# Performance work log

Hardware: AMD Instinct MI355X
Metric: run time of the kernel (lower is better)

The kernel has to match this reference:

```python
import jax, jax.numpy as jnp
import numpy as np

N, E = 50000, 800000
F_IN, F_EMB1, F_EMB2, F_HID, F_OUT = 128, 512, 128, 1024, 64


def _linear_params(k, fan_in, fan_out):
    s = 1.0 / np.sqrt(fan_in)
    kw, kb = jax.random.split(k)
    W = jax.random.uniform(kw, (fan_in, fan_out), jnp.float32, -s, s)
    b = jax.random.uniform(kb, (fan_out,), jnp.float32, -s, s)
    return W, b


def setup_inputs() -> dict:
    key = jax.random.key(0)
    ks = jax.random.split(key, 8)
    x = jax.random.normal(ks[0], (N, F_IN), jnp.float32)
    src = jax.random.randint(ks[1], (E,), 0, N)
    dst = jax.random.randint(ks[2], (E,), 0, N)
    edge_index = jnp.stack([src, dst])  # [2, E]
    edge_weight = jax.random.uniform(ks[3], (E,), jnp.float32)  # positive weights
    W1, b1 = _linear_params(ks[4], F_IN, F_EMB1)
    W2, b2 = _linear_params(ks[5], F_EMB1, F_EMB2)
    W3, b3 = _linear_params(ks[6], F_EMB2, F_HID)
    W4, b4 = _linear_params(ks[7], F_HID, F_OUT)
    return dict(x=x, edge_index=edge_index, edge_weight=edge_weight,
                W1=W1, b1=b1, W2=W2, b2=b2, W3=W3, b3=b3, W4=W4, b4=b4)


def gcn_conv(x, src, dst, w, W, b):
    """PyG GCNConv: transform, then sym-normalized weighted aggregation with self-loops.
    out = D^{-1/2} (A_w + I) D^{-1/2} (x W) + b,  deg = scatter(w @ dst) + 1."""
    n = x.shape[0]
    h = x @ W  # [N, F_out]
    deg = jax.ops.segment_sum(w, dst, num_segments=n) + 1.0  # +1 for self-loop weight
    dinv = jax.lax.rsqrt(deg)
    norm = dinv[src] * w * dinv[dst]  # [E]
    agg = jax.ops.segment_sum(norm[:, None] * h[src], dst, num_segments=n)
    agg = agg + h / deg[:, None]  # self-loop: dinv[i]*1*dinv[i] * h[i]
    return agg + b


def reference(x, edge_index, edge_weight, W1, b1, W2, b2, W3, b3, W4, b4):
    src, dst = edge_index[0], edge_index[1]
    h = jax.nn.relu(gcn_conv(x, src, dst, edge_weight, W1, b1))
    # graph_normalization=False -> identity; dropout is identity in eval mode
    h = jax.nn.relu(gcn_conv(h, src, dst, edge_weight, W2, b2))
    h = jax.nn.relu(h @ W3 + b3)
    out = jax.nn.relu(h @ W4 + b4)
    return out
```

## Files before the change

kernel.cpp:

```cpp
#include <hip/hip_runtime.h>


#define ELLW 64

typedef short bf16x8 __attribute__((ext_vector_type(8)));
typedef float f32x4 __attribute__((ext_vector_type(4)));

__device__ __forceinline__ unsigned short f2b(float f) {
    unsigned u = __builtin_bit_cast(unsigned, f);
    unsigned r = (u + 0x7FFFu + ((u >> 16) & 1u)) >> 16;
    return (unsigned short)r;
}
__device__ __forceinline__ float b2f(unsigned short u) {
    return __builtin_bit_cast(float, (unsigned)u << 16);
}

__global__ void k_setup(const float* __restrict__ x,
                        const float* __restrict__ W1, const float* __restrict__ W2,
                        const float* __restrict__ W3, const float* __restrict__ W4,
                        unsigned short* __restrict__ W1t, unsigned short* __restrict__ W2t,
                        unsigned short* __restrict__ W3t, unsigned short* __restrict__ W4t,
                        unsigned short* __restrict__ xb,
                        const int* __restrict__ src, const int* __restrict__ dst,
                        const float* __restrict__ ew, int* __restrict__ cnt,
                        int2* __restrict__ s_edge, int Nn, int E) {
    int b = blockIdx.x;
    if (b < 3125) {
        int e = b * 256 + threadIdx.x;
        if (e < E) {
            int d = dst[e];
            int2 rec = make_int2(src[e], __builtin_bit_cast(int, ew[e]));
            int slot = atomicAdd(&cnt[d], 1);
            if (slot < ELLW) s_edge[(size_t)d * ELLW + slot] = rec;
        }
    } else if (b < 4405) {
        int i = (b - 3125) * 256 + threadIdx.x;
        if (i < 65536) {
            int k = i >> 9, n = i & 511;
            W1t[n * 128 + k] = f2b(W1[i]);
        } else if (i < 131072) {
            int j = i - 65536; int k = j >> 7, n = j & 127;
            W2t[n * 512 + k] = f2b(W2[j]);
        } else if (i < 262144) {
            int j = i - 131072; int k = j >> 10, n = j & 1023;
            W3t[n * 128 + k] = f2b(W3[j]);
        } else {
            int j = i - 262144; int k = j >> 6, n = j & 63;
            W4t[n * 1024 + k] = f2b(W4[j]);
        }
    } else {
        int i = (b - 4405) * 256 + threadIdx.x;
        if (i < Nn * 32) {
            float4 v = ((const float4*)x)[i];
            ushort4 o;
            o.x = f2b(v.x); o.y = f2b(v.y); o.z = f2b(v.z); o.w = f2b(v.w);
            ((ushort4*)xb)[i] = o;
        }
    }
}

__global__ __launch_bounds__(256) void k_deg(const int2* __restrict__ s_edge,
                                             const int* __restrict__ cnt,
                                             float* __restrict__ dinv, int Nn) {
    int node = blockIdx.x * 4 + (threadIdx.x >> 6);
    if (node >= Nn) return;
    int lane = threadIdx.x & 63;
    int c = min(cnt[node], ELLW);
    float s = 0.0f;
    if (lane < c) s = __builtin_bit_cast(float, s_edge[(size_t)node * ELLW + lane].y);
    #pragma unroll
    for (int d = 32; d > 0; d >>= 1) s += __shfl_down(s, d);
    if (lane == 0) dinv[node] = rsqrtf(1.0f + s);
}

template <bool FIRST, bool BIAS_RELU>
__global__ __launch_bounds__(256) void k_gather(
    const unsigned short* __restrict__ Xb, int2* __restrict__ s_edge,
    const int* __restrict__ cnt, const float* __restrict__ dinv,
    const float* __restrict__ bias, unsigned short* __restrict__ outb, int Nn) {
    int node = blockIdx.x * 4 + (threadIdx.x >> 6);
    if (node >= Nn) return;
    int lane = threadIdx.x & 63;
    float di = dinv[node];
    float dii = di * di;
    ushort2 sv = ((const ushort2*)(Xb + (size_t)node * 128))[lane];
    float ax = b2f(sv.x) * dii, ay = b2f(sv.y) * dii;

    int c = min(cnt[node], ELLW);
    size_t base = (size_t)node * ELLW;
    int sreg = 0;
    float nv = 0.0f;
    if (lane < c) {
        int2 rec = s_edge[base + lane];
        sreg = rec.x;
        if (FIRST) {
            float wv = __builtin_bit_cast(float, rec.y);
            nv = dinv[sreg] * wv * di;
            ((int*)s_edge)[2 * (base + lane) + 1] = __builtin_bit_cast(int, nv);
        } else {
            nv = __builtin_bit_cast(float, rec.y);
        }
    }

    int j = 0;
    for (; j + 8 <= c; j += 8) {
        int s0 = __shfl(sreg, j),     s1 = __shfl(sreg, j + 1);
        int s2 = __shfl(sreg, j + 2), s3 = __shfl(sreg, j + 3);
        int s4 = __shfl(sreg, j + 4), s5 = __shfl(sreg, j + 5);
        int s6 = __shfl(sreg, j + 6), s7 = __shfl(sreg, j + 7);
        float n0 = __shfl(nv, j),     n1 = __shfl(nv, j + 1);
        float n2 = __shfl(nv, j + 2), n3 = __shfl(nv, j + 3);
        float n4 = __shfl(nv, j + 4), n5 = __shfl(nv, j + 5);
        float n6 = __shfl(nv, j + 6), n7 = __shfl(nv, j + 7);
        ushort2 r0 = ((const ushort2*)(Xb + (size_t)s0 * 128))[lane];
        ushort2 r1 = ((const ushort2*)(Xb + (size_t)s1 * 128))[lane];
        ushort2 r2 = ((const ushort2*)(Xb + (size_t)s2 * 128))[lane];
        ushort2 r3 = ((const ushort2*)(Xb + (size_t)s3 * 128))[lane];
        ushort2 r4 = ((const ushort2*)(Xb + (size_t)s4 * 128))[lane];
        ushort2 r5 = ((const ushort2*)(Xb + (size_t)s5 * 128))[lane];
        ushort2 r6 = ((const ushort2*)(Xb + (size_t)s6 * 128))[lane];
        ushort2 r7 = ((const ushort2*)(Xb + (size_t)s7 * 128))[lane];
        ax += n0 * b2f(r0.x) + n1 * b2f(r1.x) + n2 * b2f(r2.x) + n3 * b2f(r3.x);
        ay += n0 * b2f(r0.y) + n1 * b2f(r1.y) + n2 * b2f(r2.y) + n3 * b2f(r3.y);
        ax += n4 * b2f(r4.x) + n5 * b2f(r5.x) + n6 * b2f(r6.x) + n7 * b2f(r7.x);
        ay += n4 * b2f(r4.y) + n5 * b2f(r5.y) + n6 * b2f(r6.y) + n7 * b2f(r7.y);
    }
    for (; j < c; ++j) {
        int sj = __shfl(sreg, j);
        float nj = __shfl(nv, j);
        ushort2 r = ((const ushort2*)(Xb + (size_t)sj * 128))[lane];
        ax += nj * b2f(r.x);
        ay += nj * b2f(r.y);
    }

    if (BIAS_RELU) {
        float2 bv = ((const float2*)bias)[lane];
        ax = fmaxf(ax + bv.x, 0.0f);
        ay = fmaxf(ay + bv.y, 0.0f);
    }
    ushort2 o; o.x = f2b(ax); o.y = f2b(ay);
    ((ushort2*)(outb + (size_t)node * 128))[lane] = o;
}

template <int H, int OUTW, bool HAS_BO, bool OUT_BF16>
__global__ __launch_bounds__(256) void k_mlp(
    const unsigned short* __restrict__ A, const unsigned short* __restrict__ Wht,
    const unsigned short* __restrict__ Wot, const float* __restrict__ bh,
    const float* __restrict__ bo, void* __restrict__ out, int M) {
    constexpr int HC = H / 64;
    constexpr int NJ = OUTW / 16;
    constexpr int OW4 = OUTW / 32;
    __shared__ __align__(16) unsigned short Whs[64 * 128];
    __shared__ __align__(16) unsigned short Ps[128 * 64];
    __shared__ __align__(16) unsigned short Wos[OUTW * 64];
    const int tid = threadIdx.x, wave = tid >> 6, lane = tid & 63;
    const int lm = lane & 15, quad = lane >> 4;
    const int bm0 = blockIdx.x * 128;

    bf16x8 af[2][4];
    #pragma unroll
    for (int i = 0; i < 2; ++i) {
        int gr = bm0 + wave * 32 + i * 16 + lm;
        #pragma unroll
        for (int kb = 0; kb < 4; ++kb) af[i][kb] = bf16x8{0, 0, 0, 0, 0, 0, 0, 0};
        if (gr < M) {
            #pragma unroll
            for (int kb = 0; kb < 4; ++kb)
                af[i][kb] = *(const bf16x8*)(A + (size_t)gr * 128 + kb * 32 + quad * 8);
        }
    }

    #pragma unroll
    for (int u = 0; u < 4; ++u) {
        int idx = tid + u * 256; int r = idx >> 4, g = idx & 15;
        *(int4*)&Whs[r * 128 + ((g ^ (r & 15)) * 8)] =
            *(const int4*)(Wht + (size_t)r * 128 + g * 8);
    }
    #pragma unroll
    for (int u = 0; u < OW4; ++u) {
        int idx = tid + u * 256; int r = idx >> 3, g = idx & 7;
        *(int4*)&Wos[r * 64 + ((g ^ (r & 7)) * 8)] =
            *(const int4*)(Wot + (size_t)r * H + g * 8);
    }
    __syncthreads();

    f32x4 oacc[2][NJ] = {};
    for (int c = 0; c < HC; ++c) {
        f32x4 hacc[2][4] = {};
        #pragma unroll
        for (int kb = 0; kb < 4; ++kb) {
            bf16x8 bfr[4];
            #pragma unroll
            for (int j = 0; j < 4; ++j) {
                int r = j * 16 + lm, g = kb * 4 + quad;
                bfr[j] = *(const bf16x8*)&Whs[r * 128 + ((g ^ (r & 15)) * 8)];
            }
            #pragma unroll
            for (int i = 0; i < 2; ++i)
                #pragma unroll
                for (int j = 0; j < 4; ++j)
                    hacc[i][j] = __builtin_amdgcn_mfma_f32_16x16x32_bf16(
                        af[i][kb], bfr[j], hacc[i][j], 0, 0, 0);
        }

        #pragma unroll
        for (int i = 0; i < 2; ++i) {
            #pragma unroll
            for (int j = 0; j < 4; ++j) {
                int col = j * 16 + lm;
                float bv = bh[c * 64 + col];
                #pragma unroll
                for (int r4 = 0; r4 < 4; ++r4) {
                    int row = wave * 32 + i * 16 + quad * 4 + r4;
                    float o = fmaxf(hacc[i][j][r4] + bv, 0.0f);
                    Ps[row * 64 + (((col >> 3) ^ (row & 7)) * 8) + (col & 7)] = f2b(o);
                }
            }
        }

        #pragma unroll
        for (int kb = 0; kb < 2; ++kb) {
            bf16x8 pf[2];
            #pragma unroll
            for (int i = 0; i < 2; ++i) {
                int r = wave * 32 + i * 16 + lm, g = kb * 4 + quad;
                pf[i] = *(const bf16x8*)&Ps[r * 64 + ((g ^ (r & 7)) * 8)];
            }
            #pragma unroll
            for (int j = 0; j < NJ; ++j) {
                int r = j * 16 + lm, g = kb * 4 + quad;
                bf16x8 wf = *(const bf16x8*)&Wos[r * 64 + ((g ^ (r & 7)) * 8)];
                #pragma unroll
                for (int i = 0; i < 2; ++i)
                    oacc[i][j] = __builtin_amdgcn_mfma_f32_16x16x32_bf16(
                        pf[i], wf, oacc[i][j], 0, 0, 0);
            }
        }

        if (c + 1 < HC) {
            __syncthreads();
            #pragma unroll
            for (int u = 0; u < 4; ++u) {
                int idx = tid + u * 256; int r = idx >> 4, g = idx & 15;
                *(int4*)&Whs[r * 128 + ((g ^ (r & 15)) * 8)] =
                    *(const int4*)(Wht + (size_t)((c + 1) * 64 + r) * 128 + g * 8);
            }
            #pragma unroll
            for (int u = 0; u < OW4; ++u) {
                int idx = tid + u * 256; int r = idx >> 3, g = idx & 7;
                *(int4*)&Wos[r * 64 + ((g ^ (r & 7)) * 8)] =
                    *(const int4*)(Wot + (size_t)r * H + (c + 1) * 64 + g * 8);
            }
            __syncthreads();
        }
    }

    #pragma unroll
    for (int i = 0; i < 2; ++i) {
        #pragma unroll
        for (int j = 0; j < NJ; ++j) {
            int col = j * 16 + lm;
            float bv = HAS_BO ? bo[col] : 0.0f;
            #pragma unroll
            for (int r4 = 0; r4 < 4; ++r4) {
                int m = bm0 + wave * 32 + i * 16 + quad * 4 + r4;
                if (m < M) {
                    float o = oacc[i][j][r4];
                    if (HAS_BO) o = fmaxf(o + bv, 0.0f);
                    if (OUT_BF16)
                        ((unsigned short*)out)[(size_t)m * OUTW + col] = f2b(o);
                    else
                        ((float*)out)[(size_t)m * OUTW + col] = o;
                }
            }
        }
    }
}

static inline int cdiv(long a, long b) { return (int)((a + b - 1) / b); }

extern "C" void kernel_launch(void* const* d_in, const int* in_sizes, int n_in,
                              void* d_out, int out_size, void* d_ws, size_t ws_size,
                              hipStream_t stream) {
    const float* x  = (const float*)d_in[0];
    const int*   ei = (const int*)d_in[1];
    const float* ew = (const float*)d_in[2];
    const float* W1 = (const float*)d_in[3];
    const float* b1 = (const float*)d_in[4];
    const float* W2 = (const float*)d_in[5];
    const float* b2 = (const float*)d_in[6];
    const float* W3 = (const float*)d_in[7];
    const float* b3 = (const float*)d_in[8];
    const float* W4 = (const float*)d_in[9];
    const float* b4 = (const float*)d_in[10];
    const int Nn = in_sizes[0] / 128;
    const int E  = in_sizes[1] / 2;
    const int* src = ei;
    const int* dst = ei + E;

    char* ws = (char*)d_ws;
    size_t off_b = 0;
    auto alloc = [&](size_t bytes) -> void* {
        void* p = ws + off_b;
        off_b += (bytes + 255) & ~(size_t)255;
        return p;
    };
    float*          dinv   = (float*)alloc((size_t)Nn * 4);
    int*            cnt    = (int*)alloc((size_t)Nn * 4);
    int2*           s_edge = (int2*)alloc((size_t)Nn * ELLW * 8);
    unsigned short* W1t    = (unsigned short*)alloc(512 * 128 * 2);
    unsigned short* W2t    = (unsigned short*)alloc(128 * 512 * 2);
    unsigned short* W3t    = (unsigned short*)alloc(1024 * 128 * 2);
    unsigned short* W4t    = (unsigned short*)alloc(64 * 1024 * 2);
    unsigned short* xb     = (unsigned short*)alloc((size_t)Nn * 128 * 2);
    unsigned short* t2b    = (unsigned short*)alloc((size_t)Nn * 128 * 2);
    unsigned short* actb   = (unsigned short*)alloc((size_t)Nn * 128 * 2);
    float*          out    = (float*)d_out;

    hipMemsetAsync(cnt, 0, (size_t)Nn * 4, stream);
    k_setup<<<10655, 256, 0, stream>>>(x, W1, W2, W3, W4, W1t, W2t, W3t, W4t,
                                       xb, src, dst, ew, cnt, s_edge, Nn, E);
    k_deg<<<cdiv(Nn, 4), 256, 0, stream>>>(s_edge, cnt, dinv, Nn);

    k_gather<true, false><<<cdiv(Nn, 4), 256, 0, stream>>>(
        xb, s_edge, cnt, dinv, nullptr, actb, Nn);
    k_mlp<512, 128, false, true><<<cdiv(Nn, 128), 256, 0, stream>>>(
        actb, W1t, W2t, b1, nullptr, t2b, Nn);

    k_gather<false, true><<<cdiv(Nn, 4), 256, 0, stream>>>(
        t2b, s_edge, cnt, dinv, b2, actb, Nn);

    k_mlp<1024, 64, true, false><<<cdiv(Nn, 128), 256, 0, stream>>>(
        actb, W3t, W4t, b3, b4, out, Nn);
}
```

Baseline: 289.4 us.

## Factor symmetric normalization into node-side scaling and pack degree into count atomic

The edge-count atomic becomes a 64-bit atomic that also accumulates a fixed-point sum of edge weights, so the degree is available without a separate reduction over the edge lists. The D^{-1/2} factors are moved to node-side scaling: inputs are pre-scaled by dinv in a new degree/scale kernel, each gather multiplies its sum by dinv, and the first MLP scales its output by dinv. This removes the per-edge random dinv[src] lookup and the write-back of normalized weights in the first gather. The cost is an extra read-modify-write pass over xb, 64-bit atomics, fixed-point rounding of the degree, and an extra bf16 rounding of the pre-scaled input.

```diff
diff --git a/kernel.cpp b/kernel.cpp
--- a/kernel.cpp
+++ b/kernel.cpp
@@ -22,16 +22,22 @@
                         unsigned short* __restrict__ W3t, unsigned short* __restrict__ W4t,
                         unsigned short* __restrict__ xb,
                         const int* __restrict__ src, const int* __restrict__ dst,
-                        const float* __restrict__ ew, int* __restrict__ cnt,
+                        const float* __restrict__ ew,
+                        unsigned long long* __restrict__ cnt64,
                         int2* __restrict__ s_edge, int Nn, int E) {
     int b = blockIdx.x;
     if (b < 3125) {
         int e = b * 256 + threadIdx.x;
         if (e < E) {
             int d = dst[e];
-            int2 rec = make_int2(src[e], __builtin_bit_cast(int, ew[e]));
-            int slot = atomicAdd(&cnt[d], 1);
-            if (slot < ELLW) s_edge[(size_t)d * ELLW + slot] = rec;
+            float wv = ew[e];
+            unsigned wfix = (unsigned)(wv * 8388608.0f);
+            unsigned long long add = ((unsigned long long)1 << 32) | wfix;
+            unsigned long long old = atomicAdd(&cnt64[d], add);
+            int slot = (int)(old >> 32);
+            if (slot < ELLW)
+                s_edge[(size_t)d * ELLW + slot] =
+                    make_int2(src[e], __builtin_bit_cast(int, wv));
         }
     } else if (b < 4405) {
         int i = (b - 3125) * 256 + threadIdx.x;
@@ -59,47 +65,43 @@
     }
 }
 
-__global__ __launch_bounds__(256) void k_deg(const int2* __restrict__ s_edge,
-                                             const int* __restrict__ cnt,
-                                             float* __restrict__ dinv, int Nn) {
+__global__ __launch_bounds__(256) void k_degscale(
+    const unsigned long long* __restrict__ cnt64, float* __restrict__ dinv,
+    unsigned short* __restrict__ xb, int Nn) {
     int node = blockIdx.x * 4 + (threadIdx.x >> 6);
     if (node >= Nn) return;
     int lane = threadIdx.x & 63;
-    int c = min(cnt[node], ELLW);
-    float s = 0.0f;
-    if (lane < c) s = __builtin_bit_cast(float, s_edge[(size_t)node * ELLW + lane].y);
-    #pragma unroll
-    for (int d = 32; d > 0; d >>= 1) s += __shfl_down(s, d);
-    if (lane == 0) dinv[node] = rsqrtf(1.0f + s);
-}
-
-template <bool FIRST, bool BIAS_RELU>
+    unsigned long long cv = cnt64[node];
+    float deg = 1.0f + (float)(unsigned)(cv & 0xFFFFFFFFull) * (1.0f / 8388608.0f);
+    float di = rsqrtf(deg);
+    if (lane == 0) dinv[node] = di;
+    ushort2 v = ((ushort2*)(xb + (size_t)node * 128))[lane];
+    ushort2 o;
+    o.x = f2b(b2f(v.x) * di);
+    o.y = f2b(b2f(v.y) * di);
+    ((ushort2*)(xb + (size_t)node * 128))[lane] = o;
+}
+
+template <bool BIAS_RELU>
 __global__ __launch_bounds__(256) void k_gather(
-    const unsigned short* __restrict__ Xb, int2* __restrict__ s_edge,
-    const int* __restrict__ cnt, const float* __restrict__ dinv,
+    const unsigned short* __restrict__ Xb, const int2* __restrict__ s_edge,
+    const unsigned long long* __restrict__ cnt64, const float* __restrict__ dinv,
     const float* __restrict__ bias, unsigned short* __restrict__ outb, int Nn) {
     int node = blockIdx.x * 4 + (threadIdx.x >> 6);
     if (node >= Nn) return;
     int lane = threadIdx.x & 63;
     float di = dinv[node];
-    float dii = di * di;
     ushort2 sv = ((const ushort2*)(Xb + (size_t)node * 128))[lane];
-    float ax = b2f(sv.x) * dii, ay = b2f(sv.y) * dii;
-
-    int c = min(cnt[node], ELLW);
+    float ax = b2f(sv.x), ay = b2f(sv.y);
+
+    int c = min((int)(cnt64[node] >> 32), ELLW);
     size_t base = (size_t)node * ELLW;
     int sreg = 0;
     float nv = 0.0f;
     if (lane < c) {
         int2 rec = s_edge[base + lane];
         sreg = rec.x;
-        if (FIRST) {
-            float wv = __builtin_bit_cast(float, rec.y);
-            nv = dinv[sreg] * wv * di;
-            ((int*)s_edge)[2 * (base + lane) + 1] = __builtin_bit_cast(int, nv);
-        } else {
-            nv = __builtin_bit_cast(float, rec.y);
-        }
+        nv = __builtin_bit_cast(float, rec.y);
     }
 
     int j = 0;
@@ -133,6 +135,7 @@
         ay += nj * b2f(r.y);
     }
 
+    ax *= di; ay *= di;
     if (BIAS_RELU) {
         float2 bv = ((const float2*)bias)[lane];
         ax = fmaxf(ax + bv.x, 0.0f);
@@ -142,11 +145,12 @@
     ((ushort2*)(outb + (size_t)node * 128))[lane] = o;
 }
 
-template <int H, int OUTW, bool HAS_BO, bool OUT_BF16>
+template <int H, int OUTW, bool HAS_BO, bool OUT_BF16, bool SCALE_OUT>
 __global__ __launch_bounds__(256) void k_mlp(
     const unsigned short* __restrict__ A, const unsigned short* __restrict__ Wht,
     const unsigned short* __restrict__ Wot, const float* __restrict__ bh,
-    const float* __restrict__ bo, void* __restrict__ out, int M) {
+    const float* __restrict__ bo, const float* __restrict__ dinv,
+    void* __restrict__ out, int M) {
     constexpr int HC = H / 64;
     constexpr int NJ = OUTW / 16;
     constexpr int OW4 = OUTW / 32;
@@ -266,6 +270,7 @@
                 int m = bm0 + wave * 32 + i * 16 + quad * 4 + r4;
                 if (m < M) {
                     float o = oacc[i][j][r4];
+                    if (SCALE_OUT) o *= dinv[m];
                     if (HAS_BO) o = fmaxf(o + bv, 0.0f);
                     if (OUT_BF16)
                         ((unsigned short*)out)[(size_t)m * OUTW + col] = f2b(o);
@@ -305,31 +310,31 @@
         off_b += (bytes + 255) & ~(size_t)255;
         return p;
     };
-    float*          dinv   = (float*)alloc((size_t)Nn * 4);
-    int*            cnt    = (int*)alloc((size_t)Nn * 4);
-    int2*           s_edge = (int2*)alloc((size_t)Nn * ELLW * 8);
-    unsigned short* W1t    = (unsigned short*)alloc(512 * 128 * 2);
-    unsigned short* W2t    = (unsigned short*)alloc(128 * 512 * 2);
-    unsigned short* W3t    = (unsigned short*)alloc(1024 * 128 * 2);
-    unsigned short* W4t    = (unsigned short*)alloc(64 * 1024 * 2);
-    unsigned short* xb     = (unsigned short*)alloc((size_t)Nn * 128 * 2);
-    unsigned short* t2b    = (unsigned short*)alloc((size_t)Nn * 128 * 2);
-    unsigned short* actb   = (unsigned short*)alloc((size_t)Nn * 128 * 2);
-    float*          out    = (float*)d_out;
-
-    hipMemsetAsync(cnt, 0, (size_t)Nn * 4, stream);
+    float*              dinv   = (float*)alloc((size_t)Nn * 4);
+    unsigned long long* cnt64  = (unsigned long long*)alloc((size_t)Nn * 8);
+    int2*               s_edge = (int2*)alloc((size_t)Nn * ELLW * 8);
+    unsigned short*     W1t    = (unsigned short*)alloc(512 * 128 * 2);
+    unsigned short*     W2t    = (unsigned short*)alloc(128 * 512 * 2);
+    unsigned short*     W3t    = (unsigned short*)alloc(1024 * 128 * 2);
+    unsigned short*     W4t    = (unsigned short*)alloc(64 * 1024 * 2);
+    unsigned short*     xb     = (unsigned short*)alloc((size_t)Nn * 128 * 2);
+    unsigned short*     t2b    = (unsigned short*)alloc((size_t)Nn * 128 * 2);
+    unsigned short*     actb   = (unsigned short*)alloc((size_t)Nn * 128 * 2);
+    float*              out    = (float*)d_out;
+
+    hipMemsetAsync(cnt64, 0, (size_t)Nn * 8, stream);
     k_setup<<<10655, 256, 0, stream>>>(x, W1, W2, W3, W4, W1t, W2t, W3t, W4t,
-                                       xb, src, dst, ew, cnt, s_edge, Nn, E);
-    k_deg<<<cdiv(Nn, 4), 256, 0, stream>>>(s_edge, cnt, dinv, Nn);
-
-    k_gather<true, false><<<cdiv(Nn, 4), 256, 0, stream>>>(
-        xb, s_edge, cnt, dinv, nullptr, actb, Nn);
-    k_mlp<512, 128, false, true><<<cdiv(Nn, 128), 256, 0, stream>>>(
-        actb, W1t, W2t, b1, nullptr, t2b, Nn);
-
-    k_gather<false, true><<<cdiv(Nn, 4), 256, 0, stream>>>(
-        t2b, s_edge, cnt, dinv, b2, actb, Nn);
-
-    k_mlp<1024, 64, true, false><<<cdiv(Nn, 128), 256, 0, stream>>>(
-        actb, W3t, W4t, b3, b4, out, Nn);
-}
+                                       xb, src, dst, ew, cnt64, s_edge, Nn, E);
+    k_degscale<<<cdiv(Nn, 4), 256, 0, stream>>>(cnt64, dinv, xb, Nn);
+
+    k_gather<false><<<cdiv(Nn, 4), 256, 0, stream>>>(
+        xb, s_edge, cnt64, dinv, nullptr, actb, Nn);
+    k_mlp<512, 128, false, true, true><<<cdiv(Nn, 128), 256, 0, stream>>>(
+        actb, W1t, W2t, b1, nullptr, dinv, t2b, Nn);
+
+    k_gather<true><<<cdiv(Nn, 4), 256, 0, stream>>>(
+        t2b, s_edge, cnt64, dinv, b2, actb, Nn);
+
+    k_mlp<1024, 64, true, false, false><<<cdiv(Nn, 128), 256, 0, stream>>>(
+        actb, W3t, W4t, b3, b4, nullptr, out, Nn);
+}
```

After: 318.7 us. 10.1% more time.

## Split fused MLP output columns across grid y to raise parallelism

Applied to the files above, without the earlier changes.

Generalizes the fused MLP kernel to produce a 64-column slice of the output per block, using blockIdx.y to select the slice. The first MLP launch now uses two column blocks, halving per-block output accumulators and LDS for the output weights. This raises occupancy and block count. In exchange, each column block recomputes the full hidden layer, duplicating the hidden GEMM work and the loads of A and the hidden weights.

```diff
diff --git a/kernel.cpp b/kernel.cpp
--- a/kernel.cpp
+++ b/kernel.cpp
@@ -142,20 +142,19 @@
     ((ushort2*)(outb + (size_t)node * 128))[lane] = o;
 }
 
-template <int H, int OUTW, bool HAS_BO, bool OUT_BF16>
+template <int H, bool HAS_BO, bool OUT_BF16>
 __global__ __launch_bounds__(256) void k_mlp(
     const unsigned short* __restrict__ A, const unsigned short* __restrict__ Wht,
     const unsigned short* __restrict__ Wot, const float* __restrict__ bh,
-    const float* __restrict__ bo, void* __restrict__ out, int M) {
+    const float* __restrict__ bo, void* __restrict__ out, int M, int Ntot) {
     constexpr int HC = H / 64;
-    constexpr int NJ = OUTW / 16;
-    constexpr int OW4 = OUTW / 32;
     __shared__ __align__(16) unsigned short Whs[64 * 128];
     __shared__ __align__(16) unsigned short Ps[128 * 64];
-    __shared__ __align__(16) unsigned short Wos[OUTW * 64];
+    __shared__ __align__(16) unsigned short Wos[64 * 64];
     const int tid = threadIdx.x, wave = tid >> 6, lane = tid & 63;
     const int lm = lane & 15, quad = lane >> 4;
     const int bm0 = blockIdx.x * 128;
+    const int bn0 = blockIdx.y * 64;
 
     bf16x8 af[2][4];
     #pragma unroll
@@ -177,14 +176,14 @@
             *(const int4*)(Wht + (size_t)r * 128 + g * 8);
     }
     #pragma unroll
-    for (int u = 0; u < OW4; ++u) {
+    for (int u = 0; u < 2; ++u) {
         int idx = tid + u * 256; int r = idx >> 3, g = idx & 7;
         *(int4*)&Wos[r * 64 + ((g ^ (r & 7)) * 8)] =
-            *(const int4*)(Wot + (size_t)r * H + g * 8);
+            *(const int4*)(Wot + (size_t)(bn0 + r) * H + g * 8);
     }
     __syncthreads();
 
-    f32x4 oacc[2][NJ] = {};
+    f32x4 oacc[2][4] = {};
     for (int c = 0; c < HC; ++c) {
         f32x4 hacc[2][4] = {};
         #pragma unroll
@@ -227,7 +226,7 @@
                 pf[i] = *(const bf16x8*)&Ps[r * 64 + ((g ^ (r & 7)) * 8)];
             }
             #pragma unroll
-            for (int j = 0; j < NJ; ++j) {
+            for (int j = 0; j < 4; ++j) {
                 int r = j * 16 + lm, g = kb * 4 + quad;
                 bf16x8 wf = *(const bf16x8*)&Wos[r * 64 + ((g ^ (r & 7)) * 8)];
                 #pragma unroll
@@ -246,10 +245,10 @@
                     *(const int4*)(Wht + (size_t)((c + 1) * 64 + r) * 128 + g * 8);
             }
             #pragma unroll
-            for (int u = 0; u < OW4; ++u) {
+            for (int u = 0; u < 2; ++u) {
                 int idx = tid + u * 256; int r = idx >> 3, g = idx & 7;
                 *(int4*)&Wos[r * 64 + ((g ^ (r & 7)) * 8)] =
-                    *(const int4*)(Wot + (size_t)r * H + (c + 1) * 64 + g * 8);
+                    *(const int4*)(Wot + (size_t)(bn0 + r) * H + (c + 1) * 64 + g * 8);
             }
             __syncthreads();
         }
@@ -258,8 +257,8 @@
     #pragma unroll
     for (int i = 0; i < 2; ++i) {
         #pragma unroll
-        for (int j = 0; j < NJ; ++j) {
-            int col = j * 16 + lm;
+        for (int j = 0; j < 4; ++j) {
+            int col = bn0 + j * 16 + lm;
             float bv = HAS_BO ? bo[col] : 0.0f;
             #pragma unroll
             for (int r4 = 0; r4 < 4; ++r4) {
@@ -268,9 +267,9 @@
                     float o = oacc[i][j][r4];
                     if (HAS_BO) o = fmaxf(o + bv, 0.0f);
                     if (OUT_BF16)
-                        ((unsigned short*)out)[(size_t)m * OUTW + col] = f2b(o);
+                        ((unsigned short*)out)[(size_t)m * Ntot + col] = f2b(o);
                     else
-                        ((float*)out)[(size_t)m * OUTW + col] = o;
+                        ((float*)out)[(size_t)m * Ntot + col] = o;
                 }
             }
         }
@@ -324,12 +323,12 @@
 
     k_gather<true, false><<<cdiv(Nn, 4), 256, 0, stream>>>(
         xb, s_edge, cnt, dinv, nullptr, actb, Nn);
-    k_mlp<512, 128, false, true><<<cdiv(Nn, 128), 256, 0, stream>>>(
-        actb, W1t, W2t, b1, nullptr, t2b, Nn);
+    k_mlp<512, false, true><<<dim3(cdiv(Nn, 128), 2), 256, 0, stream>>>(
+        actb, W1t, W2t, b1, nullptr, t2b, Nn, 128);
 
     k_gather<false, true><<<cdiv(Nn, 4), 256, 0, stream>>>(
         t2b, s_edge, cnt, dinv, b2, actb, Nn);
 
-    k_mlp<1024, 64, true, false><<<cdiv(Nn, 128), 256, 0, stream>>>(
-        actb, W3t, W4t, b3, b4, out, Nn);
-}
+    k_mlp<1024, true, false><<<dim3(cdiv(Nn, 128), 1), 256, 0, stream>>>(
+        actb, W3t, W4t, b3, b4, out, Nn, 64);
+}
```

Result: slower. 297.7 us (+2.9%).

## Register-prefetch MLP weight chunks and pad degree counters to avoid atomic contention

Applied to the files above, without the earlier changes.

The fused MLP kernel now loads the next weight chunk into registers while the current chunk's MFMAs run, then writes it to shared memory at the start of the next iteration. This replaces the old load-then-sync pattern so global latency overlaps with compute, at the cost of extra registers; launch bounds are also changed to allow only one block. Separately, the per-node edge counters are padded to 128-byte strides so that atomics to neighbouring nodes do not share a cache line. That padding makes the counter array and its memset 32 times larger and spreads the count reads in the degree and gather kernels.

```diff
diff --git a/kernel.cpp b/kernel.cpp
--- a/kernel.cpp
+++ b/kernel.cpp
@@ -2,6 +2,7 @@
 
 
 #define ELLW 64
+#define CNTS 32
 
 typedef short bf16x8 __attribute__((ext_vector_type(8)));
 typedef float f32x4 __attribute__((ext_vector_type(4)));
@@ -30,7 +31,7 @@
         if (e < E) {
             int d = dst[e];
             int2 rec = make_int2(src[e], __builtin_bit_cast(int, ew[e]));
-            int slot = atomicAdd(&cnt[d], 1);
+            int slot = atomicAdd(&cnt[(size_t)d * CNTS], 1);
             if (slot < ELLW) s_edge[(size_t)d * ELLW + slot] = rec;
         }
     } else if (b < 4405) {
@@ -65,7 +66,7 @@
     int node = blockIdx.x * 4 + (threadIdx.x >> 6);
     if (node >= Nn) return;
     int lane = threadIdx.x & 63;
-    int c = min(cnt[node], ELLW);
+    int c = min(cnt[(size_t)node * CNTS], ELLW);
     float s = 0.0f;
     if (lane < c) s = __builtin_bit_cast(float, s_edge[(size_t)node * ELLW + lane].y);
     #pragma unroll
@@ -86,7 +87,7 @@
     ushort2 sv = ((const ushort2*)(Xb + (size_t)node * 128))[lane];
     float ax = b2f(sv.x) * dii, ay = b2f(sv.y) * dii;
 
-    int c = min(cnt[node], ELLW);
+    int c = min(cnt[(size_t)node * CNTS], ELLW);
     size_t base = (size_t)node * ELLW;
     int sreg = 0;
     float nv = 0.0f;
@@ -143,7 +144,7 @@
 }
 
 template <int H, int OUTW, bool HAS_BO, bool OUT_BF16>
-__global__ __launch_bounds__(256) void k_mlp(
+__global__ __launch_bounds__(256, 1) void k_mlp(
     const unsigned short* __restrict__ A, const unsigned short* __restrict__ Wht,
     const unsigned short* __restrict__ Wot, const float* __restrict__ bh,
     const float* __restrict__ bo, void* __restrict__ out, int M) {
@@ -170,22 +171,45 @@
         }
     }
 
+    int4 pw[4], po[OW4];
     #pragma unroll
     for (int u = 0; u < 4; ++u) {
         int idx = tid + u * 256; int r = idx >> 4, g = idx & 15;
-        *(int4*)&Whs[r * 128 + ((g ^ (r & 15)) * 8)] =
-            *(const int4*)(Wht + (size_t)r * 128 + g * 8);
+        pw[u] = *(const int4*)(Wht + (size_t)r * 128 + g * 8);
     }
     #pragma unroll
     for (int u = 0; u < OW4; ++u) {
         int idx = tid + u * 256; int r = idx >> 3, g = idx & 7;
-        *(int4*)&Wos[r * 64 + ((g ^ (r & 7)) * 8)] =
-            *(const int4*)(Wot + (size_t)r * H + g * 8);
-    }
-    __syncthreads();
+        po[u] = *(const int4*)(Wot + (size_t)r * H + g * 8);
+    }
 
     f32x4 oacc[2][NJ] = {};
     for (int c = 0; c < HC; ++c) {
+        if (c) __syncthreads();
+        #pragma unroll
+        for (int u = 0; u < 4; ++u) {
+            int idx = tid + u * 256; int r = idx >> 4, g = idx & 15;
+            *(int4*)&Whs[r * 128 + ((g ^ (r & 15)) * 8)] = pw[u];
+        }
+        #pragma unroll
+        for (int u = 0; u < OW4; ++u) {
+            int idx = tid + u * 256; int r = idx >> 3, g = idx & 7;
+            *(int4*)&Wos[r * 64 + ((g ^ (r & 7)) * 8)] = po[u];
+        }
+        __syncthreads();
+
+        const int cn = (c + 1 < HC) ? c + 1 : 0;
+        #pragma unroll
+        for (int u = 0; u < 4; ++u) {
+            int idx = tid + u * 256; int r = idx >> 4, g = idx & 15;
+            pw[u] = *(const int4*)(Wht + (size_t)(cn * 64 + r) * 128 + g * 8);
+        }
+        #pragma unroll
+        for (int u = 0; u < OW4; ++u) {
+            int idx = tid + u * 256; int r = idx >> 3, g = idx & 7;
+            po[u] = *(const int4*)(Wot + (size_t)r * H + cn * 64 + g * 8);
+        }
+
         f32x4 hacc[2][4] = {};
         #pragma unroll
         for (int kb = 0; kb < 4; ++kb) {
@@ -235,23 +259,6 @@
                     oacc[i][j] = __builtin_amdgcn_mfma_f32_16x16x32_bf16(
                         pf[i], wf, oacc[i][j], 0, 0, 0);
             }
-        }
-
-        if (c + 1 < HC) {
-            __syncthreads();
-            #pragma unroll
-            for (int u = 0; u < 4; ++u) {
-                int idx = tid + u * 256; int r = idx >> 4, g = idx & 15;
-                *(int4*)&Whs[r * 128 + ((g ^ (r & 15)) * 8)] =
-                    *(const int4*)(Wht + (size_t)((c + 1) * 64 + r) * 128 + g * 8);
-            }
-            #pragma unroll
-            for (int u = 0; u < OW4; ++u) {
-                int idx = tid + u * 256; int r = idx >> 3, g = idx & 7;
-                *(int4*)&Wos[r * 64 + ((g ^ (r & 7)) * 8)] =
-                    *(const int4*)(Wot + (size_t)r * H + (c + 1) * 64 + g * 8);
-            }
-            __syncthreads();
         }
     }
 
@@ -306,7 +313,7 @@
         return p;
     };
     float*          dinv   = (float*)alloc((size_t)Nn * 4);
-    int*            cnt    = (int*)alloc((size_t)Nn * 4);
+    int*            cnt    = (int*)alloc((size_t)Nn * CNTS * 4);
     int2*           s_edge = (int2*)alloc((size_t)Nn * ELLW * 8);
     unsigned short* W1t    = (unsigned short*)alloc(512 * 128 * 2);
     unsigned short* W2t    = (unsigned short*)alloc(128 * 512 * 2);
@@ -317,7 +324,7 @@
     unsigned short* actb   = (unsigned short*)alloc((size_t)Nn * 128 * 2);
     float*          out    = (float*)d_out;
 
-    hipMemsetAsync(cnt, 0, (size_t)Nn * 4, stream);
+    hipMemsetAsync(cnt, 0, (size_t)Nn * CNTS * 4, stream);
     k_setup<<<10655, 256, 0, stream>>>(x, W1, W2, W3, W4, W1t, W2t, W3t, W4t,
                                        xb, src, dst, ew, cnt, s_edge, Nn, E);
     k_deg<<<cdiv(Nn, 4), 256, 0, stream>>>(s_edge, cnt, dinv, Nn);
```

Result: slower. 347.5 us (+20.1%).
